# Optimization experiments

Measured on AMD Instinct MI355X. Metric: run time of the kernel, lower is better.

Reference implementation:

```python
import jax, jax.numpy as jnp
import numpy as np

B, A, R, I, V = 256, 196, 1024, 1024, 10000  # batch, att_size, rnn_size, input_size, output_size


def _lin_init(key, out_dim, in_dim):
    kw, kb = jax.random.split(key)
    s = 1.0 / np.sqrt(in_dim)
    w = jax.random.uniform(kw, (out_dim, in_dim), jnp.float32, -s, s)
    b = jax.random.uniform(kb, (out_dim,), jnp.float32, -s, s)
    return w, b


def setup_inputs() -> dict:
    key = jax.random.key(0)
    ks = jax.random.split(key, 11)
    x = jax.random.normal(ks[0], (B, I), jnp.float32)
    att = jax.random.normal(ks[1], (B, A, R), jnp.float32)
    prev_c = jax.random.normal(ks[2], (B, R), jnp.float32)
    prev_h = jax.random.normal(ks[3], (B, R), jnp.float32)
    a2a_w, a2a_b = _lin_init(ks[4], A, R)
    h2a_w, h2a_b = _lin_init(ks[5], A, R)
    d2d_w, d2d_b = _lin_init(ks[6], 1, A)
    i2h_w, i2h_b = _lin_init(ks[7], 4 * R, I)
    h2h_w, h2h_b = _lin_init(ks[8], 4 * R, R)
    r2a_w, r2a_b = _lin_init(ks[9], 4 * R, R)
    proj_w, proj_b = _lin_init(ks[10], V, R)
    return dict(x=x, att=att, prev_c=prev_c, prev_h=prev_h,
                a2a_w=a2a_w, a2a_b=a2a_b, h2a_w=h2a_w, h2a_b=h2a_b,
                d2d_w=d2d_w, d2d_b=d2d_b, i2h_w=i2h_w, i2h_b=i2h_b,
                h2h_w=h2h_w, h2h_b=h2h_b, r2a_w=r2a_w, r2a_b=r2a_b,
                proj_w=proj_w, proj_b=proj_b)


def reference(x, att, prev_c, prev_h, a2a_w, a2a_b, h2a_w, h2a_b,
              d2d_w, d2d_b, i2h_w, i2h_b, h2h_w, h2h_b,
              r2a_w, r2a_b, proj_w, proj_b):
    # Bahdanau-style attention: att [B, A, R]
    att_v = jnp.einsum('bir,ar->bia', att, a2a_w) + a2a_b      # [B, A, A]
    att_h = prev_h @ h2a_w.T + h2a_b                            # [B, A]
    dot = jnp.tanh(att_h[:, :, None] + att_v)                   # [B, A, A]
    score = jnp.einsum('bia,a->bi', dot, d2d_w[0]) + d2d_b[0]   # [B, A]
    weight = jax.nn.softmax(score, axis=1)                      # [B, A]
    att_res = jnp.einsum('bir,bi->br', att, weight)             # [B, R]
    # LSTM cell gating
    sums = (x @ i2h_w.T + i2h_b) + (prev_h @ h2h_w.T + h2h_b) + (att_res @ r2a_w.T + r2a_b)
    in_gate = jax.nn.sigmoid(sums[:, 0:R])
    forget_gate = jax.nn.sigmoid(sums[:, R:2 * R])
    out_gate = jax.nn.sigmoid(sums[:, 2 * R:3 * R])
    in_transform = jnp.tanh(sums[:, 3 * R:4 * R])
    next_c = forget_gate * prev_c + in_gate * in_transform
    next_h = out_gate * jnp.tanh(next_c)
    logsoft = jax.nn.log_softmax(next_h @ proj_w.T + proj_b, axis=1)
    return (next_c, next_h, logsoft)
```

## Files before the change

kernel.cpp:

```cpp
#include <hip/hip_runtime.h>
#include <math.h>

#define B_ 256
#define A_ 196
#define R_ 1024
#define V_ 10000
#define G4 4096
#define M_ (B_ * A_)

typedef __bf16 bf16x8 __attribute__((ext_vector_type(8)));
typedef float f32x4 __attribute__((ext_vector_type(4)));

#define OFF_ATTH   0
#define OFF_SCORE  50176
#define OFF_WEIGHT 100352
#define OFF_ATTRES 150528
#define OFF_P0     412672
#define OFF_P1     1461248
#define OFF_NHBF   2509824
#define OFF_LOGITS 2640896
#define OFF_PACKA  5200896
#define OFF_PACKH  5307392

__device__ __forceinline__ float tanh_fast(float x) {
    float e = __expf(2.f * x);
    return 1.f - 2.f / (e + 1.f);
}
__device__ __forceinline__ float sigmoid_fast(float x) {
    return 1.f / (1.f + __expf(-x));
}

__device__ __forceinline__ bf16x8 cvt8(float4 f0, float4 f1) {
    bf16x8 v;
    v[0] = (__bf16)f0.x; v[1] = (__bf16)f0.y; v[2] = (__bf16)f0.z; v[3] = (__bf16)f0.w;
    v[4] = (__bf16)f1.x; v[5] = (__bf16)f1.y; v[6] = (__bf16)f1.z; v[7] = (__bf16)f1.w;
    return v;
}

__global__ void pack_kernel(const float* __restrict__ a2a_w,
                            const float* __restrict__ h2a_w,
                            __bf16* __restrict__ packA,
                            __bf16* __restrict__ packH) {
    int row = blockIdx.x;
    int c = threadIdx.x * 4;
    if (row < 208) {
        float4 f = (row < A_) ? *(const float4*)(a2a_w + (size_t)row * R_ + c)
                              : make_float4(0.f, 0.f, 0.f, 0.f);
        __bf16* p = packA + (size_t)row * R_ + c;
        p[0] = (__bf16)f.x; p[1] = (__bf16)f.y; p[2] = (__bf16)f.z; p[3] = (__bf16)f.w;
    } else {
        int r2 = row - 208;
        float4 f = (r2 < A_) ? *(const float4*)(h2a_w + (size_t)r2 * R_ + c)
                             : make_float4(0.f, 0.f, 0.f, 0.f);
        __bf16* p = packH + (size_t)r2 * R_ + c;
        p[0] = (__bf16)f.x; p[1] = (__bf16)f.y; p[2] = (__bf16)f.z; p[3] = (__bf16)f.w;
    }
}

__global__ __launch_bounds__(256)
void att_h_gemm(const float* __restrict__ prev_h,
                const __bf16* __restrict__ packH,
                const float* __restrict__ h2a_b,
                float* __restrict__ att_h) {
    __shared__ alignas(16) __bf16 As[64][40];
    __shared__ alignas(16) __bf16 Bs[64][40];
    int tid = threadIdx.x;
    int m0 = blockIdx.x * 64, n0 = blockIdx.y * 64;
    int lane = tid & 63, w = tid >> 6, ln = lane & 15, quad = lane >> 4;
    int arow = tid >> 2, akq = (tid & 3) * 8;

    f32x4 acc[4];
#pragma unroll
    for (int t = 0; t < 4; ++t) acc[t] = {0.f, 0.f, 0.f, 0.f};

    const float* Asrc = prev_h + (size_t)(m0 + arow) * R_ + akq;
    const __bf16* Bsrc = packH + (size_t)(n0 + arow) * R_ + akq;

    float4 pa0 = *(const float4*)Asrc;
    float4 pa1 = *(const float4*)(Asrc + 4);
    bf16x8 pb = *(const bf16x8*)Bsrc;

    for (int k0 = 0; k0 < R_; k0 += 32) {
        __syncthreads();
        *(bf16x8*)&As[arow][akq] = cvt8(pa0, pa1);
        *(bf16x8*)&Bs[arow][akq] = pb;
        __syncthreads();
        if (k0 + 32 < R_) {
            pa0 = *(const float4*)(Asrc + k0 + 32);
            pa1 = *(const float4*)(Asrc + k0 + 36);
            pb = *(const bf16x8*)(Bsrc + k0 + 32);
        }
        bf16x8 a = *(bf16x8*)&As[w * 16 + ln][quad * 8];
#pragma unroll
        for (int t = 0; t < 4; ++t) {
            bf16x8 b = *(bf16x8*)&Bs[t * 16 + ln][quad * 8];
            acc[t] = __builtin_amdgcn_mfma_f32_16x16x32_bf16(a, b, acc[t], 0, 0, 0);
        }
    }
#pragma unroll
    for (int t = 0; t < 4; ++t) {
#pragma unroll
        for (int r = 0; r < 4; ++r) {
            int m = m0 + w * 16 + quad * 4 + r;
            int n = n0 + t * 16 + ln;
            if (n < A_) att_h[m * A_ + n] = acc[t][r] + h2a_b[n];
        }
    }
}

__global__ __launch_bounds__(256)
void score_gemm_mfma(const float* __restrict__ att,
                     const __bf16* __restrict__ packA,
                     const float* __restrict__ a2a_b,
                     const float* __restrict__ d2d_w,
                     const float* __restrict__ att_h,
                     float* __restrict__ score) {
    __shared__ alignas(16) __bf16 As[64][40];
    __shared__ alignas(16) __bf16 Bs[208][40];
    int tid = threadIdx.x;
    int m0 = blockIdx.x * 64;
    int lane = tid & 63, w = tid >> 6, ln = lane & 15, quad = lane >> 4;
    int arow = tid >> 2, akq = (tid & 3) * 8;

    f32x4 acc[13];
#pragma unroll
    for (int t = 0; t < 13; ++t) acc[t] = {0.f, 0.f, 0.f, 0.f};

    const float* Asrc = att + (size_t)(m0 + arow) * R_ + akq;

    float4 pa0 = *(const float4*)Asrc;
    float4 pa1 = *(const float4*)(Asrc + 4);
    bf16x8 pb[4];
#pragma unroll
    for (int i = 0; i < 4; ++i) {
        int c = tid + i * 256;
        if (c < 832) {
            int brow = c >> 2, bkq = (c & 3) * 8;
            pb[i] = *(const bf16x8*)(packA + (size_t)brow * R_ + bkq);
        }
    }

    for (int k0 = 0; k0 < R_; k0 += 32) {
        __syncthreads();
        *(bf16x8*)&As[arow][akq] = cvt8(pa0, pa1);
#pragma unroll
        for (int i = 0; i < 4; ++i) {
            int c = tid + i * 256;
            if (c < 832) {
                int brow = c >> 2, bkq = (c & 3) * 8;
                *(bf16x8*)&Bs[brow][bkq] = pb[i];
            }
        }
        __syncthreads();
        if (k0 + 32 < R_) {
            pa0 = *(const float4*)(Asrc + k0 + 32);
            pa1 = *(const float4*)(Asrc + k0 + 36);
#pragma unroll
            for (int i = 0; i < 4; ++i) {
                int c = tid + i * 256;
                if (c < 832) {
                    int brow = c >> 2, bkq = (c & 3) * 8;
                    pb[i] = *(const bf16x8*)(packA + (size_t)brow * R_ + k0 + 32 + bkq);
                }
            }
        }
        bf16x8 a = *(bf16x8*)&As[w * 16 + ln][quad * 8];
#pragma unroll
        for (int t = 0; t < 13; ++t) {
            bf16x8 b = *(bf16x8*)&Bs[t * 16 + ln][quad * 8];
            acc[t] = __builtin_amdgcn_mfma_f32_16x16x32_bf16(a, b, acc[t], 0, 0, 0);
        }
    }

    float wv[13], bb[13];
#pragma unroll
    for (int t = 0; t < 13; ++t) {
        int n = t * 16 + ln;
        wv[t] = (n < A_) ? d2d_w[n] : 0.f;
        bb[t] = (n < A_) ? a2a_b[n] : 0.f;
    }
#pragma unroll
    for (int r = 0; r < 4; ++r) {
        int m = m0 + w * 16 + quad * 4 + r;
        float ah = att_h[m];
        float p = 0.f;
#pragma unroll
        for (int t = 0; t < 13; ++t)
            p += tanh_fast(acc[t][r] + bb[t] + ah) * wv[t];
        p += __shfl_xor(p, 1);
        p += __shfl_xor(p, 2);
        p += __shfl_xor(p, 4);
        p += __shfl_xor(p, 8);
        if (ln == 0) score[m] = p;
    }
}

__global__ void softmax_kernel(const float* __restrict__ score,
                               const float* __restrict__ d2d_b,
                               float* __restrict__ weight) {
    int b = blockIdx.x;
    int i = threadIdx.x;
    __shared__ float red[256];
    float sval = 0.f;
    float s = -1e30f;
    if (i < A_) {
        sval = score[b * A_ + i] + d2d_b[0];
        s = sval;
    }
    red[i] = s; __syncthreads();
    for (int off = 128; off > 0; off >>= 1) {
        if (i < off) red[i] = fmaxf(red[i], red[i + off]);
        __syncthreads();
    }
    float mx = red[0]; __syncthreads();
    float e = (i < A_) ? __expf(sval - mx) : 0.f;
    red[i] = e; __syncthreads();
    for (int off = 128; off > 0; off >>= 1) {
        if (i < off) red[i] += red[i + off];
        __syncthreads();
    }
    float inv = 1.f / red[0];
    if (i < A_) weight[b * A_ + i] = e * inv;
}

__global__ __launch_bounds__(256)
void att_res_kernel(const float* __restrict__ att,
                    const float* __restrict__ weight,
                    float* __restrict__ att_res) {
    int b = blockIdx.x;
    int r = threadIdx.x * 4;
    __shared__ float w[A_];
    if (threadIdx.x < A_) w[threadIdx.x] = weight[b * A_ + threadIdx.x];
    __syncthreads();
    const float* ap = att + (size_t)b * A_ * R_ + r;
    float4 acc = make_float4(0.f, 0.f, 0.f, 0.f);
    for (int i = 0; i < A_; i += 4) {
        float4 v0 = *(const float4*)(ap + (size_t)(i + 0) * R_);
        float4 v1 = *(const float4*)(ap + (size_t)(i + 1) * R_);
        float4 v2 = *(const float4*)(ap + (size_t)(i + 2) * R_);
        float4 v3 = *(const float4*)(ap + (size_t)(i + 3) * R_);
        float w0 = w[i], w1 = w[i + 1], w2 = w[i + 2], w3 = w[i + 3];
        acc.x += v0.x * w0 + v1.x * w1 + v2.x * w2 + v3.x * w3;
        acc.y += v0.y * w0 + v1.y * w1 + v2.y * w2 + v3.y * w3;
        acc.z += v0.z * w0 + v1.z * w1 + v2.z * w2 + v3.z * w3;
        acc.w += v0.w * w0 + v1.w * w1 + v2.w * w2 + v3.w * w3;
    }
    *(float4*)(att_res + (size_t)b * R_ + r) = acc;
}

__global__ __launch_bounds__(256)
void sums_gemm_mfma(const float* __restrict__ x,
                    const float* __restrict__ prev_h,
                    const float* __restrict__ att_res,
                    const float* __restrict__ i2h_w,
                    const float* __restrict__ h2h_w,
                    const float* __restrict__ r2a_w,
                    float* __restrict__ P0,
                    float* __restrict__ P1) {
    __shared__ alignas(16) __bf16 As[64][40];
    __shared__ alignas(16) __bf16 Bs[64][40];
    int tid = threadIdx.x;
    int m0 = blockIdx.x * 64, n0 = blockIdx.y * 64;
    int ks = blockIdx.z;
    int kbeg = ks * 512, kend = kbeg + 512;
    int lane = tid & 63, w = tid >> 6, ln = lane & 15, quad = lane >> 4;
    int arow = tid >> 2, akq = (tid & 3) * 8;

    f32x4 acc[4];
#pragma unroll
    for (int t = 0; t < 4; ++t) acc[t] = {0.f, 0.f, 0.f, 0.f};

    const float* Al[3] = {x, prev_h, att_res};
    const float* Bl[3] = {i2h_w, h2h_w, r2a_w};
    for (int p = 0; p < 3; ++p) {
        const float* Asrc = Al[p] + (size_t)(m0 + arow) * R_ + akq;
        const float* Bsrc = Bl[p] + (size_t)(n0 + arow) * R_ + akq;
        float4 pa0 = *(const float4*)(Asrc + kbeg);
        float4 pa1 = *(const float4*)(Asrc + kbeg + 4);
        float4 pb0 = *(const float4*)(Bsrc + kbeg);
        float4 pb1 = *(const float4*)(Bsrc + kbeg + 4);
        for (int k0 = kbeg; k0 < kend; k0 += 32) {
            __syncthreads();
            *(bf16x8*)&As[arow][akq] = cvt8(pa0, pa1);
            *(bf16x8*)&Bs[arow][akq] = cvt8(pb0, pb1);
            __syncthreads();
            if (k0 + 32 < kend) {
                pa0 = *(const float4*)(Asrc + k0 + 32);
                pa1 = *(const float4*)(Asrc + k0 + 36);
                pb0 = *(const float4*)(Bsrc + k0 + 32);
                pb1 = *(const float4*)(Bsrc + k0 + 36);
            }
            bf16x8 a = *(bf16x8*)&As[w * 16 + ln][quad * 8];
#pragma unroll
            for (int t = 0; t < 4; ++t) {
                bf16x8 b = *(bf16x8*)&Bs[t * 16 + ln][quad * 8];
                acc[t] = __builtin_amdgcn_mfma_f32_16x16x32_bf16(a, b, acc[t], 0, 0, 0);
            }
        }
    }
    float* P = ks ? P1 : P0;
#pragma unroll
    for (int t = 0; t < 4; ++t) {
#pragma unroll
        for (int r = 0; r < 4; ++r) {
            int m = m0 + w * 16 + quad * 4 + r;
            int n = n0 + t * 16 + ln;
            P[(size_t)m * G4 + n] = acc[t][r];
        }
    }
}

__global__ void gates_kernel(const float* __restrict__ P0,
                             const float* __restrict__ P1,
                             const float* __restrict__ i2h_b,
                             const float* __restrict__ h2h_b,
                             const float* __restrict__ r2a_b,
                             const float* __restrict__ prev_c,
                             float* __restrict__ out_c,
                             float* __restrict__ out_h,
                             __bf16* __restrict__ nh_bf) {
    int idx = blockIdx.x * 256 + threadIdx.x;
    int b = idx >> 10, r = idx & 1023;
    size_t off = (size_t)b * G4;
    float s0 = P0[off + r] + P1[off + r] + i2h_b[r] + h2h_b[r] + r2a_b[r];
    float s1 = P0[off + R_ + r] + P1[off + R_ + r] + i2h_b[R_ + r] + h2h_b[R_ + r] + r2a_b[R_ + r];
    float s2 = P0[off + 2 * R_ + r] + P1[off + 2 * R_ + r] + i2h_b[2 * R_ + r] + h2h_b[2 * R_ + r] + r2a_b[2 * R_ + r];
    float s3 = P0[off + 3 * R_ + r] + P1[off + 3 * R_ + r] + i2h_b[3 * R_ + r] + h2h_b[3 * R_ + r] + r2a_b[3 * R_ + r];
    float ig = sigmoid_fast(s0);
    float fg = sigmoid_fast(s1);
    float og = sigmoid_fast(s2);
    float it = tanh_fast(s3);
    float nc = fg * prev_c[idx] + ig * it;
    float nh = og * tanh_fast(nc);
    out_c[idx] = nc;
    out_h[idx] = nh;
    nh_bf[idx] = (__bf16)nh;
}

__global__ __launch_bounds__(256)
void proj_gemm_mfma(const __bf16* __restrict__ nh_bf,
                    const float* __restrict__ proj_w,
                    const float* __restrict__ proj_b,
                    float* __restrict__ logits) {
    __shared__ alignas(16) __bf16 As[64][40];
    __shared__ alignas(16) __bf16 Bs[64][40];
    int tid = threadIdx.x;
    int m0 = blockIdx.x * 64, n0 = blockIdx.y * 64;
    int lane = tid & 63, w = tid >> 6, ln = lane & 15, quad = lane >> 4;
    int arow = tid >> 2, akq = (tid & 3) * 8;

    f32x4 acc[4];
#pragma unroll
    for (int t = 0; t < 4; ++t) acc[t] = {0.f, 0.f, 0.f, 0.f};

    int nr = n0 + arow;
    int nrc = nr < V_ ? nr : V_ - 1;
    const __bf16* Asrc = nh_bf + (size_t)(m0 + arow) * R_ + akq;
    const float* Bsrc = proj_w + (size_t)nrc * R_ + akq;

    bf16x8 pa = *(const bf16x8*)Asrc;
    float4 pb0 = *(const float4*)Bsrc;
    float4 pb1 = *(const float4*)(Bsrc + 4);

    for (int k0 = 0; k0 < R_; k0 += 32) {
        __syncthreads();
        *(bf16x8*)&As[arow][akq] = pa;
        *(bf16x8*)&Bs[arow][akq] = cvt8(pb0, pb1);
        __syncthreads();
        if (k0 + 32 < R_) {
            pa = *(const bf16x8*)(Asrc + k0 + 32);
            pb0 = *(const float4*)(Bsrc + k0 + 32);
            pb1 = *(const float4*)(Bsrc + k0 + 36);
        }
        bf16x8 a = *(bf16x8*)&As[w * 16 + ln][quad * 8];
#pragma unroll
        for (int t = 0; t < 4; ++t) {
            bf16x8 b = *(bf16x8*)&Bs[t * 16 + ln][quad * 8];
            acc[t] = __builtin_amdgcn_mfma_f32_16x16x32_bf16(a, b, acc[t], 0, 0, 0);
        }
    }
#pragma unroll
    for (int t = 0; t < 4; ++t) {
#pragma unroll
        for (int r = 0; r < 4; ++r) {
            int m = m0 + w * 16 + quad * 4 + r;
            int n = n0 + t * 16 + ln;
            if (n < V_) logits[(size_t)m * V_ + n] = acc[t][r] + proj_b[n];
        }
    }
}

__global__ void logsoftmax_kernel(const float* __restrict__ logits,
                                  float* __restrict__ out) {
    int b = blockIdx.x, t = threadIdx.x;
    __shared__ float red[256];
    const float* lp = logits + (size_t)b * V_;
    float mx = -1e30f;
    for (int v = t; v < V_; v += 256) mx = fmaxf(mx, lp[v]);
    red[t] = mx; __syncthreads();
    for (int off = 128; off > 0; off >>= 1) {
        if (t < off) red[t] = fmaxf(red[t], red[t + off]);
        __syncthreads();
    }
    mx = red[0]; __syncthreads();
    float s = 0.f;
    for (int v = t; v < V_; v += 256) s += __expf(lp[v] - mx);
    red[t] = s; __syncthreads();
    for (int off = 128; off > 0; off >>= 1) {
        if (t < off) red[t] += red[t + off];
        __syncthreads();
    }
    float lse = mx + __logf(red[0]);
    float* op = out + (size_t)b * V_;
    for (int v = t; v < V_; v += 256) op[v] = lp[v] - lse;
}

extern "C" void kernel_launch(void* const* d_in, const int* in_sizes, int n_in,
                              void* d_out, int out_size, void* d_ws, size_t ws_size,
                              hipStream_t stream) {
    const float* x      = (const float*)d_in[0];
    const float* att    = (const float*)d_in[1];
    const float* prev_c = (const float*)d_in[2];
    const float* prev_h = (const float*)d_in[3];
    const float* a2a_w  = (const float*)d_in[4];
    const float* a2a_b  = (const float*)d_in[5];
    const float* h2a_w  = (const float*)d_in[6];
    const float* h2a_b  = (const float*)d_in[7];
    const float* d2d_w  = (const float*)d_in[8];
    const float* d2d_b  = (const float*)d_in[9];
    const float* i2h_w  = (const float*)d_in[10];
    const float* i2h_b  = (const float*)d_in[11];
    const float* h2h_w  = (const float*)d_in[12];
    const float* h2h_b  = (const float*)d_in[13];
    const float* r2a_w  = (const float*)d_in[14];
    const float* r2a_b  = (const float*)d_in[15];
    const float* proj_w = (const float*)d_in[16];
    const float* proj_b = (const float*)d_in[17];

    float* ws      = (float*)d_ws;
    float* att_h   = ws + OFF_ATTH;
    float* score   = ws + OFF_SCORE;
    float* weight  = ws + OFF_WEIGHT;
    float* att_res = ws + OFF_ATTRES;
    float* P0      = ws + OFF_P0;
    float* P1      = ws + OFF_P1;
    __bf16* nh_bf  = (__bf16*)(ws + OFF_NHBF);
    float* logits  = ws + OFF_LOGITS;
    __bf16* packA  = (__bf16*)(ws + OFF_PACKA);
    __bf16* packH  = (__bf16*)(ws + OFF_PACKH);
    float* out     = (float*)d_out;

    pack_kernel<<<464, 256, 0, stream>>>(a2a_w, h2a_w, packA, packH);
    att_h_gemm<<<dim3(B_ / 64, 4), 256, 0, stream>>>(prev_h, packH, h2a_b, att_h);
    score_gemm_mfma<<<M_ / 64, 256, 0, stream>>>(att, packA, a2a_b, d2d_w, att_h, score);
    softmax_kernel<<<B_, 256, 0, stream>>>(score, d2d_b, weight);
    att_res_kernel<<<B_, 256, 0, stream>>>(att, weight, att_res);
    sums_gemm_mfma<<<dim3(B_ / 64, G4 / 64, 2), 256, 0, stream>>>(
        x, prev_h, att_res, i2h_w, h2h_w, r2a_w, P0, P1);
    gates_kernel<<<(B_ * R_) / 256, 256, 0, stream>>>(
        P0, P1, i2h_b, h2h_b, r2a_b, prev_c, out, out + B_ * R_, nh_bf);
    proj_gemm_mfma<<<dim3(B_ / 64, (V_ + 63) / 64), 256, 0, stream>>>(
        nh_bf, proj_w, proj_b, logits);
    logsoftmax_kernel<<<B_, 256, 0, stream>>>(logits, out + 2 * B_ * R_);
}
```

Measured before the change: 558.1 us.

## Stream score GEMM B tiles via async global_load_lds double buffer; split att_res

The score GEMM now loads the packed a2a weight tile straight into a double-buffered LDS region with global_load_lds, prefetching two K-steps ahead, and manual vmcnt waits and barriers take the place of the register-staged copy and two syncthreads per step. The att operand is no longer staged through LDS: each lane loads its own A fragment from global memory and converts it to bf16 in registers. Separately, att_res is split across two blocks per batch row, each thread doing float2 work, to double the number of blocks. The hand-written waitcnt counts and raw s_barrier placement are fragile and could race if the compiler reorders memory operations.

```diff
diff --git a/kernel.cpp b/kernel.cpp
--- a/kernel.cpp
+++ b/kernel.cpp
@@ -115,61 +115,75 @@
                      const float* __restrict__ d2d_w,
                      const float* __restrict__ att_h,
                      float* __restrict__ score) {
-    __shared__ alignas(16) __bf16 As[64][40];
-    __shared__ alignas(16) __bf16 Bs[208][40];
+    __shared__ alignas(16) char Bs[2][20480];
     int tid = threadIdx.x;
     int m0 = blockIdx.x * 64;
     int lane = tid & 63, w = tid >> 6, ln = lane & 15, quad = lane >> 4;
-    int arow = tid >> 2, akq = (tid & 3) * 8;
+
+    const char* packAb = (const char*)packA;
+    unsigned goff[5], loff[5];
+#pragma unroll
+    for (int j = 0; j < 5; ++j) {
+        unsigned o = (unsigned)((w * 5 + j) * 1024 + lane * 16);
+        unsigned row = o / 80u;
+        unsigned ci = (o % 80u) / 16u;
+        loff[j] = o;
+        goff[j] = (row < 208u && ci < 4u) ? (row * 2048u + ci * 16u) : 0u;
+    }
+
+    const float* Ap = att + (size_t)(m0 + w * 16 + ln) * R_ + quad * 8;
 
     f32x4 acc[13];
 #pragma unroll
     for (int t = 0; t < 13; ++t) acc[t] = {0.f, 0.f, 0.f, 0.f};
 
-    const float* Asrc = att + (size_t)(m0 + arow) * R_ + akq;
-
-    float4 pa0 = *(const float4*)Asrc;
-    float4 pa1 = *(const float4*)(Asrc + 4);
-    bf16x8 pb[4];
-#pragma unroll
-    for (int i = 0; i < 4; ++i) {
-        int c = tid + i * 256;
-        if (c < 832) {
-            int brow = c >> 2, bkq = (c & 3) * 8;
-            pb[i] = *(const bf16x8*)(packA + (size_t)brow * R_ + bkq);
-        }
-    }
-
-    for (int k0 = 0; k0 < R_; k0 += 32) {
-        __syncthreads();
-        *(bf16x8*)&As[arow][akq] = cvt8(pa0, pa1);
-#pragma unroll
-        for (int i = 0; i < 4; ++i) {
-            int c = tid + i * 256;
-            if (c < 832) {
-                int brow = c >> 2, bkq = (c & 3) * 8;
-                *(bf16x8*)&Bs[brow][bkq] = pb[i];
-            }
-        }
-        __syncthreads();
-        if (k0 + 32 < R_) {
-            pa0 = *(const float4*)(Asrc + k0 + 32);
-            pa1 = *(const float4*)(Asrc + k0 + 36);
-#pragma unroll
-            for (int i = 0; i < 4; ++i) {
-                int c = tid + i * 256;
-                if (c < 832) {
-                    int brow = c >> 2, bkq = (c & 3) * 8;
-                    pb[i] = *(const bf16x8*)(packA + (size_t)brow * R_ + k0 + 32 + bkq);
-                }
-            }
-        }
-        bf16x8 a = *(bf16x8*)&As[w * 16 + ln][quad * 8];
+#pragma unroll
+    for (int j = 0; j < 5; ++j)
+        __builtin_amdgcn_global_load_lds(
+            (const __attribute__((address_space(1))) void*)(packAb + goff[j]),
+            (__attribute__((address_space(3))) void*)(&Bs[0][0] + loff[j]), 16, 0, 0);
+    asm volatile("" ::: "memory");
+    float4 c0 = *(const float4*)Ap;
+    float4 c1 = *(const float4*)(Ap + 4);
+    asm volatile("" ::: "memory");
+#pragma unroll
+    for (int j = 0; j < 5; ++j)
+        __builtin_amdgcn_global_load_lds(
+            (const __attribute__((address_space(1))) void*)(packAb + goff[j] + 64),
+            (__attribute__((address_space(3))) void*)(&Bs[1][0] + loff[j]), 16, 0, 0);
+    asm volatile("" ::: "memory");
+
+    for (int p = 0; p < 32; ++p) {
+        int cur = p & 1;
+        const char* bufc = &Bs[cur][0];
+        float4 n0 = c0, n1 = c1;
+        if (p + 1 < 32) {
+            n0 = *(const float4*)(Ap + (p + 1) * 32);
+            n1 = *(const float4*)(Ap + (p + 1) * 32 + 4);
+        }
+        if (p + 1 < 32)
+            asm volatile("s_waitcnt vmcnt(7)" ::: "memory");
+        else
+            asm volatile("s_waitcnt vmcnt(0)" ::: "memory");
+        bf16x8 a = cvt8(c0, c1);
+        asm volatile("s_barrier" ::: "memory");
+        const char* bp = bufc + ln * 80 + quad * 16;
 #pragma unroll
         for (int t = 0; t < 13; ++t) {
-            bf16x8 b = *(bf16x8*)&Bs[t * 16 + ln][quad * 8];
+            bf16x8 b = *(const bf16x8*)(bp + t * 1280);
             acc[t] = __builtin_amdgcn_mfma_f32_16x16x32_bf16(a, b, acc[t], 0, 0, 0);
         }
+        c0 = n0; c1 = n1;
+        asm volatile("s_barrier" ::: "memory");
+        if (p + 2 < 32) {
+            unsigned kb = (unsigned)(p + 2) * 64u;
+#pragma unroll
+            for (int j = 0; j < 5; ++j)
+                __builtin_amdgcn_global_load_lds(
+                    (const __attribute__((address_space(1))) void*)(packAb + goff[j] + kb),
+                    (__attribute__((address_space(3))) void*)(bufc + loff[j]), 16, 0, 0);
+        }
+        asm volatile("" ::: "memory");
     }
 
     float wv[13], bb[13];
@@ -228,24 +242,22 @@
                     const float* __restrict__ weight,
                     float* __restrict__ att_res) {
     int b = blockIdx.x;
-    int r = threadIdx.x * 4;
-    __shared__ float w[A_];
-    if (threadIdx.x < A_) w[threadIdx.x] = weight[b * A_ + threadIdx.x];
+    int r = blockIdx.y * 512 + threadIdx.x * 2;
+    __shared__ float wsm[A_];
+    if (threadIdx.x < A_) wsm[threadIdx.x] = weight[b * A_ + threadIdx.x];
     __syncthreads();
     const float* ap = att + (size_t)b * A_ * R_ + r;
-    float4 acc = make_float4(0.f, 0.f, 0.f, 0.f);
+    float acx = 0.f, acy = 0.f;
     for (int i = 0; i < A_; i += 4) {
-        float4 v0 = *(const float4*)(ap + (size_t)(i + 0) * R_);
-        float4 v1 = *(const float4*)(ap + (size_t)(i + 1) * R_);
-        float4 v2 = *(const float4*)(ap + (size_t)(i + 2) * R_);
-        float4 v3 = *(const float4*)(ap + (size_t)(i + 3) * R_);
-        float w0 = w[i], w1 = w[i + 1], w2 = w[i + 2], w3 = w[i + 3];
-        acc.x += v0.x * w0 + v1.x * w1 + v2.x * w2 + v3.x * w3;
-        acc.y += v0.y * w0 + v1.y * w1 + v2.y * w2 + v3.y * w3;
-        acc.z += v0.z * w0 + v1.z * w1 + v2.z * w2 + v3.z * w3;
-        acc.w += v0.w * w0 + v1.w * w1 + v2.w * w2 + v3.w * w3;
-    }
-    *(float4*)(att_res + (size_t)b * R_ + r) = acc;
+        float2 v0 = *(const float2*)(ap + (size_t)(i + 0) * R_);
+        float2 v1 = *(const float2*)(ap + (size_t)(i + 1) * R_);
+        float2 v2 = *(const float2*)(ap + (size_t)(i + 2) * R_);
+        float2 v3 = *(const float2*)(ap + (size_t)(i + 3) * R_);
+        float w0 = wsm[i], w1 = wsm[i + 1], w2 = wsm[i + 2], w3 = wsm[i + 3];
+        acx += v0.x * w0 + v1.x * w1 + v2.x * w2 + v3.x * w3;
+        acy += v0.y * w0 + v1.y * w1 + v2.y * w2 + v3.y * w3;
+    }
+    *(float2*)(att_res + (size_t)b * R_ + r) = make_float2(acx, acy);
 }
 
 __global__ __launch_bounds__(256)
@@ -454,7 +466,7 @@
     att_h_gemm<<<dim3(B_ / 64, 4), 256, 0, stream>>>(prev_h, packH, h2a_b, att_h);
     score_gemm_mfma<<<M_ / 64, 256, 0, stream>>>(att, packA, a2a_b, d2d_w, att_h, score);
     softmax_kernel<<<B_, 256, 0, stream>>>(score, d2d_b, weight);
-    att_res_kernel<<<B_, 256, 0, stream>>>(att, weight, att_res);
+    att_res_kernel<<<dim3(B_, 2), 256, 0, stream>>>(att, weight, att_res);
     sums_gemm_mfma<<<dim3(B_ / 64, G4 / 64, 2), 256, 0, stream>>>(
         x, prev_h, att_res, i2h_w, h2h_w, r2a_w, P0, P1);
     gates_kernel<<<(B_ * R_) / 256, 256, 0, stream>>>(
```

Result: slower. 570.9 us (+2.3%).
